# Kernel tuning notes

Hardware: AMD Instinct MI355X
Metric: run time of the kernel (lower is better)

The kernel has to match this reference:

```python
import jax, jax.numpy as jnp
import numpy as np

N_NODES = 50000
N_EDGES = 100000
TOKENS = 10000
D = 32
EDGE_TYPES = 8
STEPS = 5


def setup_inputs() -> dict:
    key = jax.random.key(0)
    ks = jax.random.split(key, 12)
    token = jax.random.randint(ks[0], (N_NODES,), 0, TOKENS)
    etype = jax.random.randint(ks[1], (N_EDGES,), 0, EDGE_TYPES)
    src = jax.random.randint(ks[2], (N_EDGES,), 0, N_NODES)
    dst = jax.random.randint(ks[3], (N_EDGES,), 0, N_NODES)
    s = 1.0 / np.sqrt(D)
    emb = jax.random.normal(ks[4], (TOKENS, D), jnp.float32)
    # per-edge-type weights: [T, D, D, 2] (fwd/reverse message transforms)
    W_edge = jax.random.normal(ks[5], (EDGE_TYPES, D, D, 2), jnp.float32) * s
    W_r = jax.random.normal(ks[6], (3 * D, D), jnp.float32) * s
    b_r = jnp.zeros((D,), jnp.float32)
    W_z = jax.random.normal(ks[7], (3 * D, D), jnp.float32) * s
    b_z = jnp.zeros((D,), jnp.float32)
    W_t = jax.random.normal(ks[8], (3 * D, D), jnp.float32) * s
    b_t = jnp.zeros((D,), jnp.float32)
    return {"token": token, "etype": etype, "src": src, "dst": dst,
            "emb": emb, "W_edge": W_edge, "W_r": W_r, "b_r": b_r,
            "W_z": W_z, "b_z": b_z, "W_t": W_t, "b_t": b_t}


def reference(token, etype, src, dst, emb, W_edge, W_r, b_r, W_z, b_z, W_t, b_t):
    n = token.shape[0]
    prop = emb[token]                       # [N, D]
    We = W_edge[etype]                      # [E, D, D, 2] gathered per edge (once)
    for _ in range(STEPS):
        h_src = prop[src]                   # [E, D] gather source states
        # src_mul_edge + sum over src dim == per-edge matmul: [E,D,2]
        fea = jnp.einsum('ei,eijk->ejk', h_src, We)
        in_fea = jax.ops.segment_sum(fea[:, :, 0], dst, num_segments=n)   # [N, D]
        out_fea = jax.ops.segment_sum(fea[:, :, 1], src, num_segments=n)  # [N, D]
        cat = jnp.concatenate([in_fea, out_fea, prop], axis=1)            # [N, 3D]
        r = jax.nn.sigmoid(cat @ W_r + b_r)
        z = jax.nn.sigmoid(cat @ W_z + b_z)
        cat2 = jnp.concatenate([in_fea, out_fea, r * prop], axis=1)
        h_hat = jnp.tanh(cat2 @ W_t + b_t)
        prop = (1.0 - z) * prop + z * h_hat
    return prop
```

## Files before the change

kernel.cpp:

```cpp
#include <hip/hip_runtime.h>

#define N_NODES 50000
#define N_EDGES 100000
#define DD 32
#define STEPS 5
#define ETYPES 8
#define CAP_T 13312
#define CAP (ETYPES * CAP_T)
#define TRASH N_EDGES
#define SCAN_B 49

#define GRU_GRID ((N_NODES / 16 + 3) / 4)

typedef float f32x4v __attribute__((ext_vector_type(4)));
typedef short s16x8 __attribute__((ext_vector_type(8)));

__device__ __forceinline__ ushort f2bf(float x) {
    unsigned u = __float_as_uint(x);
    u += 0x7fff + ((u >> 16) & 1);
    return (ushort)(u >> 16);
}
__device__ __forceinline__ float bf2f(ushort h) {
    return __uint_as_float(((unsigned)h) << 16);
}
__device__ __forceinline__ void mk_split(const float* v, s16x8& h, s16x8& lo) {
#pragma unroll
    for (int i = 0; i < 8; ++i) {
        ushort hi = f2bf(v[i]);
        h[i] = (short)hi;
        lo[i] = (short)f2bf(v[i] - bf2f(hi));
    }
}
__device__ __forceinline__ float sigm(float x) {
    return 1.f / (1.f + __expf(-x));
}
__device__ __forceinline__ float fast_tanh(float x) {
    x = fminf(fmaxf(x, -15.f), 15.f);
    float e = __expf(2.f * x);
    return (e - 1.f) / (e + 1.f);
}

__global__ void init_kernel(const int* __restrict__ token,
                            const float* __restrict__ emb,
                            float* __restrict__ prop,
                            int* __restrict__ cnt,
                            int* __restrict__ se,
                            int* __restrict__ spi,
                            int* __restrict__ spo) {
    int idx = blockIdx.x * 256 + threadIdx.x;
    int n = idx >> 5, j = idx & 31;
    prop[idx] = emb[token[n] * DD + j];
    if (idx < 2 * N_NODES + ETYPES) cnt[idx] = 0;
    if (idx < CAP) { se[idx] = 0; spi[idx] = TRASH; spo[idx] = TRASH; }
}

__global__ __launch_bounds__(256) void
wfrag_kernel(const float* __restrict__ W_edge,
             ushort* __restrict__ wfh, ushort* __restrict__ wfl) {
    int idx = blockIdx.x * 256 + threadIdx.x;
    if (idx >= ETYPES * 4 * 64) return;
    int t  = idx >> 8;
    int nt = (idx >> 6) & 3;
    int l  = idx & 63;
    int n  = nt * 16 + (l & 15);
    int j  = n & 31;
    int p  = n >> 5;
#pragma unroll
    for (int i = 0; i < 8; ++i) {
        int k = (l >> 4) * 8 + i;
        float v = W_edge[(((size_t)t * DD + k) * DD + j) * 2 + p];
        ushort hi = f2bf(v);
        int o = ((t * 4 + nt) * 64 + l) * 8 + i;
        wfh[o] = hi;
        wfl[o] = f2bf(v - bf2f(hi));
    }
}

__global__ __launch_bounds__(256) void
wgfrag_kernel(const float* __restrict__ W_r, const float* __restrict__ W_z,
              const float* __restrict__ W_t,
              ushort* __restrict__ wgh, ushort* __restrict__ wgl) {
    int idx = blockIdx.x * 256 + threadIdx.x;
    if (idx >= 1152) return;
    int g  = idx / 384;
    int kt = (idx / 128) % 3;
    int nt = (idx / 64) % 2;
    int l  = idx & 63;
    const float* W = g == 0 ? W_r : (g == 1 ? W_z : W_t);
    int col = nt * 16 + (l & 15);
#pragma unroll
    for (int i = 0; i < 8; ++i) {
        int k = kt * 32 + (l >> 4) * 8 + i;
        float v = W[k * DD + col];
        ushort hi = f2bf(v);
        int o = (((g * 3 + kt) * 2 + nt) * 64 + l) * 8 + i;
        wgh[o] = hi;
        wgl[o] = f2bf(v - bf2f(hi));
    }
}

__global__ void hist_kernel(const int* __restrict__ etype,
                            const int* __restrict__ src,
                            const int* __restrict__ dst,
                            int* __restrict__ cnt_in, int* __restrict__ cnt_out,
                            int* __restrict__ tcnt,
                            int* __restrict__ rank_in, int* __restrict__ rank_out,
                            int* __restrict__ qe) {
    __shared__ int lh[ETYPES], lbase[ETYPES];
    int tid = threadIdx.x;
    int e = blockIdx.x * 256 + tid;
    if (tid < ETYPES) lh[tid] = 0;
    __syncthreads();
    int t = 0, lr = 0;
    bool v = e < N_EDGES;
    if (v) {
        t = etype[e];
        lr = atomicAdd(&lh[t], 1);
        rank_in[e]  = atomicAdd(&cnt_in[dst[e]], 1);
        rank_out[e] = atomicAdd(&cnt_out[src[e]], 1);
    }
    __syncthreads();
    if (tid < ETYPES) lbase[tid] = atomicAdd(&tcnt[tid], lh[tid]);
    __syncthreads();
    if (v) qe[e] = t * CAP_T + lbase[t] + lr;
}

__global__ __launch_bounds__(1024) void
scan1(const int* __restrict__ cnt_in, const int* __restrict__ cnt_out,
      int* __restrict__ off_in, int* __restrict__ off_out,
      int* __restrict__ bsum) {
    __shared__ int s[1024];
    int b = blockIdx.x;
    int ab = (b < SCAN_B) ? b : b - SCAN_B;
    const int* a = (b < SCAN_B) ? cnt_in : cnt_out;
    int* o = (b < SCAN_B) ? off_in : off_out;
    int i = ab * 1024 + threadIdx.x;
    int x = (i < N_NODES) ? a[i] : 0;
    s[threadIdx.x] = x;
    __syncthreads();
    for (int ofs = 1; ofs < 1024; ofs <<= 1) {
        int u = (threadIdx.x >= ofs) ? s[threadIdx.x - ofs] : 0;
        __syncthreads();
        s[threadIdx.x] += u;
        __syncthreads();
    }
    if (i < N_NODES) o[i] = s[threadIdx.x] - x;
    if (threadIdx.x == 1023) bsum[b] = s[1023];
}

__global__ void scan2(const int* __restrict__ bsum, int* __restrict__ ebase,
                      int* __restrict__ off_in, int* __restrict__ off_out) {
    __shared__ int s[128];
    int t = threadIdx.x;
    int x = (t < 2 * SCAN_B) ? bsum[t] : 0;
    s[t] = x;
    __syncthreads();
    for (int ofs = 1; ofs < 128; ofs <<= 1) {
        int u = (t >= ofs) ? s[t - ofs] : 0;
        __syncthreads();
        s[t] += u;
        __syncthreads();
    }
    if (t < SCAN_B) ebase[t] = s[t] - x;
    else if (t < 2 * SCAN_B) ebase[t] = s[t] - x - N_EDGES;
    if (t == 0) { off_in[N_NODES] = N_EDGES; off_out[N_NODES] = N_EDGES; }
}

__global__ __launch_bounds__(1024) void
scan3(int* __restrict__ off_in, int* __restrict__ off_out,
      const int* __restrict__ ebase) {
    int b = blockIdx.x;
    int ab = (b < SCAN_B) ? b : b - SCAN_B;
    int* o = (b < SCAN_B) ? off_in : off_out;
    int i = ab * 1024 + threadIdx.x;
    if (i < N_NODES) o[i] += ebase[b];
}

__global__ void place_kernel(const int* __restrict__ src,
                             const int* __restrict__ dst,
                             const int* __restrict__ in_off,
                             const int* __restrict__ out_off,
                             const int* __restrict__ rank_in,
                             const int* __restrict__ rank_out,
                             const int* __restrict__ qe,
                             int* __restrict__ se, int* __restrict__ spi,
                             int* __restrict__ spo) {
    int e = blockIdx.x * 256 + threadIdx.x;
    if (e < N_EDGES) {
        int q = qe[e];
        int pi = in_off[dst[e]]  + rank_in[e];
        int po = out_off[src[e]] + rank_out[e];
        if (q < CAP) {
            se[q]  = src[e];
            spi[q] = pi;
            spo[q] = po;
        }
    }
}

__global__ __launch_bounds__(256) void
edge_kernel(const int* __restrict__ se, const int* __restrict__ spi,
            const int* __restrict__ spo,
            const ushort* __restrict__ wfh, const ushort* __restrict__ wfl,
            const float* __restrict__ prop,
            float* __restrict__ fea_in, float* __restrict__ fea_out) {
    int wv = blockIdx.x * 4 + (threadIdx.x >> 6);
    int l  = threadIdx.x & 63;
    int slot0 = wv * 16;
    int type = slot0 / CAP_T;
    int m  = l & 15;
    int kb = l >> 4;

    int sm = se[slot0 + m];
    const float4* p4 = (const float4*)prop;
    float4 h0 = p4[(size_t)sm * 8 + kb * 2];
    float4 h1 = p4[(size_t)sm * 8 + kb * 2 + 1];
    float hv[8] = {h0.x, h0.y, h0.z, h0.w, h1.x, h1.y, h1.z, h1.w};
    s16x8 ah, al;
    mk_split(hv, ah, al);

    int pr[4], qr[4];
#pragma unroll
    for (int reg = 0; reg < 4; ++reg) {
        pr[reg] = spi[slot0 + kb * 4 + reg];
        qr[reg] = spo[slot0 + kb * 4 + reg];
    }

    const s16x8* bh8 = (const s16x8*)wfh;
    const s16x8* bl8 = (const s16x8*)wfl;
    f32x4v acc[4];
#pragma unroll
    for (int nt = 0; nt < 4; ++nt) {
        s16x8 bh = bh8[(type * 4 + nt) * 64 + l];
        s16x8 bl = bl8[(type * 4 + nt) * 64 + l];
        f32x4v a = {0.f, 0.f, 0.f, 0.f};
        a = __builtin_amdgcn_mfma_f32_16x16x32_bf16(ah, bh, a, 0, 0, 0);
        a = __builtin_amdgcn_mfma_f32_16x16x32_bf16(al, bh, a, 0, 0, 0);
        a = __builtin_amdgcn_mfma_f32_16x16x32_bf16(ah, bl, a, 0, 0, 0);
        acc[nt] = a;
    }

    int col = l & 15;
#pragma unroll
    for (int nt = 0; nt < 4; ++nt) {
        float* base = (nt < 2) ? fea_in : fea_out;
        int cofs = (nt & 1) * 16 + col;
#pragma unroll
        for (int reg = 0; reg < 4; ++reg) {
            int row = (nt < 2) ? pr[reg] : qr[reg];
            base[(size_t)row * DD + cofs] = acc[nt][reg];
        }
    }
}

__global__ __launch_bounds__(256) void
gru_kernel(const ushort* __restrict__ wgh, const ushort* __restrict__ wgl,
           const float* __restrict__ b_r, const float* __restrict__ b_z,
           const float* __restrict__ b_t,
           const float* __restrict__ fea_in,
           const float* __restrict__ fea_out,
           const int* __restrict__ in_off,
           const int* __restrict__ out_off,
           float* __restrict__ prop,
           float* __restrict__ out2) {
    __shared__ float tr[4][16 * 36];
    const int wvl = threadIdx.x >> 6;
    const int wv = blockIdx.x * 4 + wvl;
    if (wv * 16 >= N_NODES) return;
    const int l = threadIdx.x & 63;
    const int m = l & 15;
    const int kb = l >> 4;
    const int gn = wv * 16 + m;

    float va[8], vb[8], pA[8];
    {
        const float4* p4 = (const float4*)prop;
        float4 a = p4[(size_t)gn * 8 + kb * 2];
        float4 b = p4[(size_t)gn * 8 + kb * 2 + 1];
        pA[0] = a.x; pA[1] = a.y; pA[2] = a.z; pA[3] = a.w;
        pA[4] = b.x; pA[5] = b.y; pA[6] = b.z; pA[7] = b.w;
#pragma unroll
        for (int i = 0; i < 8; ++i) { va[i] = 0.f; vb[i] = 0.f; }
        const float4* fi4 = (const float4*)fea_in;
        const float4* fo4 = (const float4*)fea_out;
        int i0 = in_off[gn], i1 = in_off[gn + 1];
        for (int r = i0; r < i1; ++r) {
            float4 x = fi4[(size_t)r * 8 + kb * 2];
            float4 y = fi4[(size_t)r * 8 + kb * 2 + 1];
            va[0] += x.x; va[1] += x.y; va[2] += x.z; va[3] += x.w;
            va[4] += y.x; va[5] += y.y; va[6] += y.z; va[7] += y.w;
        }
        int o0 = out_off[gn], o1 = out_off[gn + 1];
        for (int r = o0; r < o1; ++r) {
            float4 x = fo4[(size_t)r * 8 + kb * 2];
            float4 y = fo4[(size_t)r * 8 + kb * 2 + 1];
            vb[0] += x.x; vb[1] += x.y; vb[2] += x.z; vb[3] += x.w;
            vb[4] += y.x; vb[5] += y.y; vb[6] += y.z; vb[7] += y.w;
        }
    }
    s16x8 ah[3], al[3];
    mk_split(va, ah[0], al[0]);
    mk_split(vb, ah[1], al[1]);
    mk_split(pA, ah[2], al[2]);

    const s16x8* bh8 = (const s16x8*)wgh;
    const s16x8* bl8 = (const s16x8*)wgl;
    f32x4v ar[2], az[2], at_[2];
#pragma unroll
    for (int nt = 0; nt < 2; ++nt) {
        ar[nt] = (f32x4v){0.f, 0.f, 0.f, 0.f};
        az[nt] = (f32x4v){0.f, 0.f, 0.f, 0.f};
        at_[nt] = (f32x4v){0.f, 0.f, 0.f, 0.f};
    }
#pragma unroll
    for (int nt = 0; nt < 2; ++nt) {
#pragma unroll
        for (int kt = 0; kt < 3; ++kt) {
            s16x8 bh = bh8[((0 * 3 + kt) * 2 + nt) * 64 + l];
            s16x8 bl = bl8[((0 * 3 + kt) * 2 + nt) * 64 + l];
            ar[nt] = __builtin_amdgcn_mfma_f32_16x16x32_bf16(ah[kt], bh, ar[nt], 0, 0, 0);
            ar[nt] = __builtin_amdgcn_mfma_f32_16x16x32_bf16(al[kt], bh, ar[nt], 0, 0, 0);
            ar[nt] = __builtin_amdgcn_mfma_f32_16x16x32_bf16(ah[kt], bl, ar[nt], 0, 0, 0);
            s16x8 ch = bh8[((1 * 3 + kt) * 2 + nt) * 64 + l];
            s16x8 cl = bl8[((1 * 3 + kt) * 2 + nt) * 64 + l];
            az[nt] = __builtin_amdgcn_mfma_f32_16x16x32_bf16(ah[kt], ch, az[nt], 0, 0, 0);
            az[nt] = __builtin_amdgcn_mfma_f32_16x16x32_bf16(al[kt], ch, az[nt], 0, 0, 0);
            az[nt] = __builtin_amdgcn_mfma_f32_16x16x32_bf16(ah[kt], cl, az[nt], 0, 0, 0);
            if (kt < 2) {
                s16x8 th = bh8[((2 * 3 + kt) * 2 + nt) * 64 + l];
                s16x8 tl = bl8[((2 * 3 + kt) * 2 + nt) * 64 + l];
                at_[nt] = __builtin_amdgcn_mfma_f32_16x16x32_bf16(ah[kt], th, at_[nt], 0, 0, 0);
                at_[nt] = __builtin_amdgcn_mfma_f32_16x16x32_bf16(al[kt], th, at_[nt], 0, 0, 0);
                at_[nt] = __builtin_amdgcn_mfma_f32_16x16x32_bf16(ah[kt], tl, at_[nt], 0, 0, 0);
            }
        }
    }

    float rv[2][4], zv[2][4], pD[2][4];
#pragma unroll
    for (int nt = 0; nt < 2; ++nt) {
        float br = b_r[nt * 16 + m];
        float bz = b_z[nt * 16 + m];
#pragma unroll
        for (int reg = 0; reg < 4; ++reg) {
            int nd = wv * 16 + kb * 4 + reg;
            pD[nt][reg] = prop[(size_t)nd * DD + nt * 16 + m];
            rv[nt][reg] = sigm(ar[nt][reg] + br) * pD[nt][reg];
            zv[nt][reg] = sigm(az[nt][reg] + bz);
        }
    }

    float* T = tr[wvl];
#pragma unroll
    for (int nt = 0; nt < 2; ++nt)
#pragma unroll
        for (int reg = 0; reg < 4; ++reg)
            T[(kb * 4 + reg) * 36 + nt * 16 + m] = rv[nt][reg];
    float rpA[8];
    {
        const float4* T4 = (const float4*)(T + m * 36 + kb * 8);
        float4 x = T4[0], y = T4[1];
        rpA[0] = x.x; rpA[1] = x.y; rpA[2] = x.z; rpA[3] = x.w;
        rpA[4] = y.x; rpA[5] = y.y; rpA[6] = y.z; rpA[7] = y.w;
    }
    s16x8 rh, rl;
    mk_split(rpA, rh, rl);
#pragma unroll
    for (int nt = 0; nt < 2; ++nt) {
        s16x8 th = bh8[((2 * 3 + 2) * 2 + nt) * 64 + l];
        s16x8 tl = bl8[((2 * 3 + 2) * 2 + nt) * 64 + l];
        at_[nt] = __builtin_amdgcn_mfma_f32_16x16x32_bf16(rh, th, at_[nt], 0, 0, 0);
        at_[nt] = __builtin_amdgcn_mfma_f32_16x16x32_bf16(rl, th, at_[nt], 0, 0, 0);
        at_[nt] = __builtin_amdgcn_mfma_f32_16x16x32_bf16(rh, tl, at_[nt], 0, 0, 0);
    }

#pragma unroll
    for (int nt = 0; nt < 2; ++nt) {
        float bt = b_t[nt * 16 + m];
#pragma unroll
        for (int reg = 0; reg < 4; ++reg) {
            int nd = wv * 16 + kb * 4 + reg;
            float tv = fast_tanh(at_[nt][reg] + bt);
            float o = fmaf(zv[nt][reg], tv - pD[nt][reg], pD[nt][reg]);
            if (out2) out2[(size_t)nd * DD + nt * 16 + m] = o;
            else      prop[(size_t)nd * DD + nt * 16 + m] = o;
        }
    }
}

extern "C" void kernel_launch(void* const* d_in, const int* in_sizes, int n_in,
                              void* d_out, int out_size, void* d_ws, size_t ws_size,
                              hipStream_t stream) {
    const int*   token  = (const int*)d_in[0];
    const int*   etype  = (const int*)d_in[1];
    const int*   src    = (const int*)d_in[2];
    const int*   dst    = (const int*)d_in[3];
    const float* emb    = (const float*)d_in[4];
    const float* W_edge = (const float*)d_in[5];
    const float* W_r    = (const float*)d_in[6];
    const float* b_r    = (const float*)d_in[7];
    const float* W_z    = (const float*)d_in[8];
    const float* b_z    = (const float*)d_in[9];
    const float* W_t    = (const float*)d_in[10];
    const float* b_t    = (const float*)d_in[11];
    float* out = (float*)d_out;

    float* prop    = (float*)d_ws;
    float* fea_in  = prop    + (size_t)N_NODES * DD;
    float* fea_out = fea_in  + (size_t)(N_EDGES + 1) * DD;
    ushort* wfh = (ushort*)(fea_out + (size_t)(N_EDGES + 1) * DD);
    ushort* wfl = wfh + ETYPES * 4 * 64 * 8;
    ushort* wgh = wfl + ETYPES * 4 * 64 * 8;
    ushort* wgl = wgh + 1152 * 8;
    int* in_off   = (int*)(wgl + 1152 * 8);
    int* out_off  = in_off + (N_NODES + 1);
    int* se       = out_off + (N_NODES + 1);
    int* spi      = se + CAP;
    int* spo      = spi + CAP;

    int* cnt      = (int*)fea_in;
    int* cnt_in   = cnt;
    int* cnt_out  = cnt + N_NODES;
    int* tcnt     = cnt + 2 * N_NODES;
    int* rank_in  = cnt + 2 * N_NODES + ETYPES;
    int* rank_out = rank_in + N_EDGES;
    int* qe       = rank_out + N_EDGES;
    int* bsum     = qe + N_EDGES;
    int* ebase    = bsum + 2 * SCAN_B;

    init_kernel<<<(N_NODES * DD) / 256, 256, 0, stream>>>(token, emb, prop, cnt,
                                                          se, spi, spo);
    wfrag_kernel<<<8, 256, 0, stream>>>(W_edge, wfh, wfl);
    wgfrag_kernel<<<5, 256, 0, stream>>>(W_r, W_z, W_t, wgh, wgl);
    hist_kernel<<<(N_EDGES + 255) / 256, 256, 0, stream>>>(
        etype, src, dst, cnt_in, cnt_out, tcnt, rank_in, rank_out, qe);
    scan1<<<2 * SCAN_B, 1024, 0, stream>>>(cnt_in, cnt_out, in_off, out_off, bsum);
    scan2<<<1, 128, 0, stream>>>(bsum, ebase, in_off, out_off);
    scan3<<<2 * SCAN_B, 1024, 0, stream>>>(in_off, out_off, ebase);
    place_kernel<<<(N_EDGES + 255) / 256, 256, 0, stream>>>(
        src, dst, in_off, out_off, rank_in, rank_out, qe, se, spi, spo);

    for (int step = 0; step < STEPS; ++step) {
        edge_kernel<<<CAP / 64, 256, 0, stream>>>(se, spi, spo, wfh, wfl, prop,
                                                  fea_in, fea_out);
        gru_kernel<<<GRU_GRID, 256, 0, stream>>>(
            wgh, wgl, b_r, b_z, b_t, fea_in, fea_out, in_off, out_off,
            prop, (step == STEPS - 1) ? out : nullptr);
    }
}
```

Baseline: 243.6 us.

## Compute outgoing messages per node from per-type out-degree counts instead of per edge

After: 240.5 us. Within noise of the previous version (-1.3%).

```diff
diff --git a/kernel.cpp b/kernel.cpp
--- a/kernel.cpp
+++ b/kernel.cpp
@@ -14,6 +14,7 @@
 
 typedef float f32x4v __attribute__((ext_vector_type(4)));
 typedef short s16x8 __attribute__((ext_vector_type(8)));
+typedef unsigned long long u64;
 
 __device__ __forceinline__ ushort f2bf(float x) {
     unsigned u = __float_as_uint(x);
@@ -44,68 +45,66 @@
                             const float* __restrict__ emb,
                             float* __restrict__ prop,
                             int* __restrict__ cnt,
+                            u64* __restrict__ c8,
                             int* __restrict__ se,
-                            int* __restrict__ spi,
-                            int* __restrict__ spo) {
+                            int* __restrict__ spi) {
     int idx = blockIdx.x * 256 + threadIdx.x;
     int n = idx >> 5, j = idx & 31;
     prop[idx] = emb[token[n] * DD + j];
-    if (idx < 2 * N_NODES + ETYPES) cnt[idx] = 0;
-    if (idx < CAP) { se[idx] = 0; spi[idx] = TRASH; spo[idx] = TRASH; }
+    if (idx < N_NODES + ETYPES) cnt[idx] = 0;
+    if (idx < N_NODES) c8[idx] = 0ull;
+    if (idx < CAP) { se[idx] = 0; spi[idx] = TRASH; }
 }
 
 __global__ __launch_bounds__(256) void
 wfrag_kernel(const float* __restrict__ W_edge,
-             ushort* __restrict__ wfh, ushort* __restrict__ wfl) {
+             const float* __restrict__ W_r, const float* __restrict__ W_z,
+             const float* __restrict__ W_t,
+             ushort* __restrict__ wfh, ushort* __restrict__ wfl,
+             ushort* __restrict__ wgh, ushort* __restrict__ wgl) {
     int idx = blockIdx.x * 256 + threadIdx.x;
-    if (idx >= ETYPES * 4 * 64) return;
-    int t  = idx >> 8;
-    int nt = (idx >> 6) & 3;
-    int l  = idx & 63;
-    int n  = nt * 16 + (l & 15);
-    int j  = n & 31;
-    int p  = n >> 5;
-#pragma unroll
-    for (int i = 0; i < 8; ++i) {
-        int k = (l >> 4) * 8 + i;
-        float v = W_edge[(((size_t)t * DD + k) * DD + j) * 2 + p];
-        ushort hi = f2bf(v);
-        int o = ((t * 4 + nt) * 64 + l) * 8 + i;
-        wfh[o] = hi;
-        wfl[o] = f2bf(v - bf2f(hi));
-    }
-}
-
-__global__ __launch_bounds__(256) void
-wgfrag_kernel(const float* __restrict__ W_r, const float* __restrict__ W_z,
-              const float* __restrict__ W_t,
-              ushort* __restrict__ wgh, ushort* __restrict__ wgl) {
-    int idx = blockIdx.x * 256 + threadIdx.x;
-    if (idx >= 1152) return;
-    int g  = idx / 384;
-    int kt = (idx / 128) % 3;
-    int nt = (idx / 64) % 2;
-    int l  = idx & 63;
-    const float* W = g == 0 ? W_r : (g == 1 ? W_z : W_t);
-    int col = nt * 16 + (l & 15);
-#pragma unroll
-    for (int i = 0; i < 8; ++i) {
-        int k = kt * 32 + (l >> 4) * 8 + i;
-        float v = W[k * DD + col];
-        ushort hi = f2bf(v);
-        int o = (((g * 3 + kt) * 2 + nt) * 64 + l) * 8 + i;
-        wgh[o] = hi;
-        wgl[o] = f2bf(v - bf2f(hi));
+    if (idx < ETYPES * 4 * 64) {
+        int t  = idx >> 8;
+        int nt = (idx >> 6) & 3;
+        int l  = idx & 63;
+        int n  = nt * 16 + (l & 15);
+        int j  = n & 31;
+        int p  = n >> 5;
+#pragma unroll
+        for (int i = 0; i < 8; ++i) {
+            int k = (l >> 4) * 8 + i;
+            float v = W_edge[(((size_t)t * DD + k) * DD + j) * 2 + p];
+            ushort hi = f2bf(v);
+            int o = ((t * 4 + nt) * 64 + l) * 8 + i;
+            wfh[o] = hi;
+            wfl[o] = f2bf(v - bf2f(hi));
+        }
+    } else if (idx < ETYPES * 4 * 64 + 1152) {
+        int x = idx - ETYPES * 4 * 64;
+        int g  = x / 384;
+        int kt = (x / 128) % 3;
+        int nt = (x / 64) % 2;
+        int l  = x & 63;
+        const float* W = g == 0 ? W_r : (g == 1 ? W_z : W_t);
+        int col = nt * 16 + (l & 15);
+#pragma unroll
+        for (int i = 0; i < 8; ++i) {
+            int k = kt * 32 + (l >> 4) * 8 + i;
+            float v = W[k * DD + col];
+            ushort hi = f2bf(v);
+            int o = (((g * 3 + kt) * 2 + nt) * 64 + l) * 8 + i;
+            wgh[o] = hi;
+            wgl[o] = f2bf(v - bf2f(hi));
+        }
     }
 }
 
 __global__ void hist_kernel(const int* __restrict__ etype,
                             const int* __restrict__ src,
                             const int* __restrict__ dst,
-                            int* __restrict__ cnt_in, int* __restrict__ cnt_out,
-                            int* __restrict__ tcnt,
-                            int* __restrict__ rank_in, int* __restrict__ rank_out,
-                            int* __restrict__ qe) {
+                            int* __restrict__ cnt_in, int* __restrict__ tcnt,
+                            u64* __restrict__ c8,
+                            int* __restrict__ rank_in, int* __restrict__ qe) {
     __shared__ int lh[ETYPES], lbase[ETYPES];
     int tid = threadIdx.x;
     int e = blockIdx.x * 256 + tid;
@@ -116,8 +115,8 @@
     if (v) {
         t = etype[e];
         lr = atomicAdd(&lh[t], 1);
-        rank_in[e]  = atomicAdd(&cnt_in[dst[e]], 1);
-        rank_out[e] = atomicAdd(&cnt_out[src[e]], 1);
+        rank_in[e] = atomicAdd(&cnt_in[dst[e]], 1);
+        atomicAdd(&c8[src[e]], 1ull << (8 * t));
     }
     __syncthreads();
     if (tid < ETYPES) lbase[tid] = atomicAdd(&tcnt[tid], lh[tid]);
@@ -126,16 +125,11 @@
 }
 
 __global__ __launch_bounds__(1024) void
-scan1(const int* __restrict__ cnt_in, const int* __restrict__ cnt_out,
-      int* __restrict__ off_in, int* __restrict__ off_out,
+scan1(const int* __restrict__ cnt_in, int* __restrict__ off_in,
       int* __restrict__ bsum) {
     __shared__ int s[1024];
-    int b = blockIdx.x;
-    int ab = (b < SCAN_B) ? b : b - SCAN_B;
-    const int* a = (b < SCAN_B) ? cnt_in : cnt_out;
-    int* o = (b < SCAN_B) ? off_in : off_out;
-    int i = ab * 1024 + threadIdx.x;
-    int x = (i < N_NODES) ? a[i] : 0;
+    int i = blockIdx.x * 1024 + threadIdx.x;
+    int x = (i < N_NODES) ? cnt_in[i] : 0;
     s[threadIdx.x] = x;
     __syncthreads();
     for (int ofs = 1; ofs < 1024; ofs <<= 1) {
@@ -144,66 +138,54 @@
         s[threadIdx.x] += u;
         __syncthreads();
     }
-    if (i < N_NODES) o[i] = s[threadIdx.x] - x;
-    if (threadIdx.x == 1023) bsum[b] = s[1023];
+    if (i < N_NODES) off_in[i] = s[threadIdx.x] - x;
+    if (threadIdx.x == 1023) bsum[blockIdx.x] = s[1023];
 }
 
 __global__ void scan2(const int* __restrict__ bsum, int* __restrict__ ebase,
-                      int* __restrict__ off_in, int* __restrict__ off_out) {
-    __shared__ int s[128];
+                      int* __restrict__ off_in) {
+    __shared__ int s[64];
     int t = threadIdx.x;
-    int x = (t < 2 * SCAN_B) ? bsum[t] : 0;
+    int x = (t < SCAN_B) ? bsum[t] : 0;
     s[t] = x;
     __syncthreads();
-    for (int ofs = 1; ofs < 128; ofs <<= 1) {
+    for (int ofs = 1; ofs < 64; ofs <<= 1) {
         int u = (t >= ofs) ? s[t - ofs] : 0;
         __syncthreads();
         s[t] += u;
         __syncthreads();
     }
     if (t < SCAN_B) ebase[t] = s[t] - x;
-    else if (t < 2 * SCAN_B) ebase[t] = s[t] - x - N_EDGES;
-    if (t == 0) { off_in[N_NODES] = N_EDGES; off_out[N_NODES] = N_EDGES; }
+    if (t == 0) off_in[N_NODES] = N_EDGES;
 }
 
 __global__ __launch_bounds__(1024) void
-scan3(int* __restrict__ off_in, int* __restrict__ off_out,
-      const int* __restrict__ ebase) {
-    int b = blockIdx.x;
-    int ab = (b < SCAN_B) ? b : b - SCAN_B;
-    int* o = (b < SCAN_B) ? off_in : off_out;
-    int i = ab * 1024 + threadIdx.x;
-    if (i < N_NODES) o[i] += ebase[b];
+scan3(int* __restrict__ off_in, const int* __restrict__ ebase) {
+    int i = blockIdx.x * 1024 + threadIdx.x;
+    if (i < N_NODES) off_in[i] += ebase[blockIdx.x];
 }
 
 __global__ void place_kernel(const int* __restrict__ src,
                              const int* __restrict__ dst,
                              const int* __restrict__ in_off,
-                             const int* __restrict__ out_off,
                              const int* __restrict__ rank_in,
-                             const int* __restrict__ rank_out,
                              const int* __restrict__ qe,
-                             int* __restrict__ se, int* __restrict__ spi,
-                             int* __restrict__ spo) {
+                             int* __restrict__ se, int* __restrict__ spi) {
     int e = blockIdx.x * 256 + threadIdx.x;
     if (e < N_EDGES) {
         int q = qe[e];
-        int pi = in_off[dst[e]]  + rank_in[e];
-        int po = out_off[src[e]] + rank_out[e];
         if (q < CAP) {
             se[q]  = src[e];
-            spi[q] = pi;
-            spo[q] = po;
+            spi[q] = in_off[dst[e]] + rank_in[e];
         }
     }
 }
 
 __global__ __launch_bounds__(256) void
 edge_kernel(const int* __restrict__ se, const int* __restrict__ spi,
-            const int* __restrict__ spo,
             const ushort* __restrict__ wfh, const ushort* __restrict__ wfl,
             const float* __restrict__ prop,
-            float* __restrict__ fea_in, float* __restrict__ fea_out) {
+            float* __restrict__ fea_in) {
     int wv = blockIdx.x * 4 + (threadIdx.x >> 6);
     int l  = threadIdx.x & 63;
     int slot0 = wv * 16;
@@ -219,18 +201,15 @@
     s16x8 ah, al;
     mk_split(hv, ah, al);
 
-    int pr[4], qr[4];
-#pragma unroll
-    for (int reg = 0; reg < 4; ++reg) {
-        pr[reg] = spi[slot0 + kb * 4 + reg];
-        qr[reg] = spo[slot0 + kb * 4 + reg];
-    }
+    int pr[4];
+#pragma unroll
+    for (int reg = 0; reg < 4; ++reg) pr[reg] = spi[slot0 + kb * 4 + reg];
 
     const s16x8* bh8 = (const s16x8*)wfh;
     const s16x8* bl8 = (const s16x8*)wfl;
-    f32x4v acc[4];
-#pragma unroll
-    for (int nt = 0; nt < 4; ++nt) {
+    f32x4v acc[2];
+#pragma unroll
+    for (int nt = 0; nt < 2; ++nt) {
         s16x8 bh = bh8[(type * 4 + nt) * 64 + l];
         s16x8 bl = bl8[(type * 4 + nt) * 64 + l];
         f32x4v a = {0.f, 0.f, 0.f, 0.f};
@@ -239,28 +218,21 @@
         a = __builtin_amdgcn_mfma_f32_16x16x32_bf16(ah, bl, a, 0, 0, 0);
         acc[nt] = a;
     }
-
-    int col = l & 15;
-#pragma unroll
-    for (int nt = 0; nt < 4; ++nt) {
-        float* base = (nt < 2) ? fea_in : fea_out;
-        int cofs = (nt & 1) * 16 + col;
-#pragma unroll
-        for (int reg = 0; reg < 4; ++reg) {
-            int row = (nt < 2) ? pr[reg] : qr[reg];
-            base[(size_t)row * DD + cofs] = acc[nt][reg];
-        }
-    }
+#pragma unroll
+    for (int nt = 0; nt < 2; ++nt)
+#pragma unroll
+        for (int reg = 0; reg < 4; ++reg)
+            fea_in[(size_t)pr[reg] * DD + nt * 16 + m] = acc[nt][reg];
 }
 
 __global__ __launch_bounds__(256) void
 gru_kernel(const ushort* __restrict__ wgh, const ushort* __restrict__ wgl,
+           const ushort* __restrict__ wfh, const ushort* __restrict__ wfl,
            const float* __restrict__ b_r, const float* __restrict__ b_z,
            const float* __restrict__ b_t,
            const float* __restrict__ fea_in,
-           const float* __restrict__ fea_out,
            const int* __restrict__ in_off,
-           const int* __restrict__ out_off,
+           const u64* __restrict__ c8,
            float* __restrict__ prop,
            float* __restrict__ out2) {
     __shared__ float tr[4][16 * 36];
@@ -272,7 +244,7 @@
     const int kb = l >> 4;
     const int gn = wv * 16 + m;
 
-    float va[8], vb[8], pA[8];
+    float va[8], pA[8];
     {
         const float4* p4 = (const float4*)prop;
         float4 a = p4[(size_t)gn * 8 + kb * 2];
@@ -280,9 +252,8 @@
         pA[0] = a.x; pA[1] = a.y; pA[2] = a.z; pA[3] = a.w;
         pA[4] = b.x; pA[5] = b.y; pA[6] = b.z; pA[7] = b.w;
 #pragma unroll
-        for (int i = 0; i < 8; ++i) { va[i] = 0.f; vb[i] = 0.f; }
+        for (int i = 0; i < 8; ++i) va[i] = 0.f;
         const float4* fi4 = (const float4*)fea_in;
-        const float4* fo4 = (const float4*)fea_out;
         int i0 = in_off[gn], i1 = in_off[gn + 1];
         for (int r = i0; r < i1; ++r) {
             float4 x = fi4[(size_t)r * 8 + kb * 2];
@@ -290,18 +261,57 @@
             va[0] += x.x; va[1] += x.y; va[2] += x.z; va[3] += x.w;
             va[4] += y.x; va[5] += y.y; va[6] += y.z; va[7] += y.w;
         }
-        int o0 = out_off[gn], o1 = out_off[gn + 1];
-        for (int r = o0; r < o1; ++r) {
-            float4 x = fo4[(size_t)r * 8 + kb * 2];
-            float4 y = fo4[(size_t)r * 8 + kb * 2 + 1];
-            vb[0] += x.x; vb[1] += x.y; vb[2] += x.z; vb[3] += x.w;
-            vb[4] += y.x; vb[5] += y.y; vb[6] += y.z; vb[7] += y.w;
-        }
-    }
+    }
+    s16x8 ph, pl;
+    mk_split(pA, ph, pl);
+
+    u64 cb[4];
+#pragma unroll
+    for (int reg = 0; reg < 4; ++reg) cb[reg] = c8[wv * 16 + kb * 4 + reg];
+    const s16x8* eh8 = (const s16x8*)wfh;
+    const s16x8* el8 = (const s16x8*)wfl;
+    f32x4v outD[2];
+    outD[0] = (f32x4v){0.f, 0.f, 0.f, 0.f};
+    outD[1] = (f32x4v){0.f, 0.f, 0.f, 0.f};
+#pragma unroll 1
+    for (int t = 0; t < ETYPES; ++t) {
+        s16x8 bh2 = eh8[(t * 4 + 2) * 64 + l];
+        s16x8 bl2 = el8[(t * 4 + 2) * 64 + l];
+        s16x8 bh3 = eh8[(t * 4 + 3) * 64 + l];
+        s16x8 bl3 = el8[(t * 4 + 3) * 64 + l];
+        f32x4v a0 = {0.f, 0.f, 0.f, 0.f}, a1 = {0.f, 0.f, 0.f, 0.f};
+        a0 = __builtin_amdgcn_mfma_f32_16x16x32_bf16(ph, bh2, a0, 0, 0, 0);
+        a0 = __builtin_amdgcn_mfma_f32_16x16x32_bf16(pl, bh2, a0, 0, 0, 0);
+        a0 = __builtin_amdgcn_mfma_f32_16x16x32_bf16(ph, bl2, a0, 0, 0, 0);
+        a1 = __builtin_amdgcn_mfma_f32_16x16x32_bf16(ph, bh3, a1, 0, 0, 0);
+        a1 = __builtin_amdgcn_mfma_f32_16x16x32_bf16(pl, bh3, a1, 0, 0, 0);
+        a1 = __builtin_amdgcn_mfma_f32_16x16x32_bf16(ph, bl3, a1, 0, 0, 0);
+#pragma unroll
+        for (int reg = 0; reg < 4; ++reg) {
+            float w = (float)((cb[reg] >> (8 * t)) & 0xff);
+            outD[0][reg] = fmaf(w, a0[reg], outD[0][reg]);
+            outD[1][reg] = fmaf(w, a1[reg], outD[1][reg]);
+        }
+    }
+
+    float* T = tr[wvl];
+#pragma unroll
+    for (int nt = 0; nt < 2; ++nt)
+#pragma unroll
+        for (int reg = 0; reg < 4; ++reg)
+            T[(kb * 4 + reg) * 36 + nt * 16 + m] = outD[nt][reg];
+    float oA[8];
+    {
+        const float4* T4 = (const float4*)(T + m * 36 + kb * 8);
+        float4 x = T4[0], y = T4[1];
+        oA[0] = x.x; oA[1] = x.y; oA[2] = x.z; oA[3] = x.w;
+        oA[4] = y.x; oA[5] = y.y; oA[6] = y.z; oA[7] = y.w;
+    }
+
     s16x8 ah[3], al[3];
     mk_split(va, ah[0], al[0]);
-    mk_split(vb, ah[1], al[1]);
-    mk_split(pA, ah[2], al[2]);
+    mk_split(oA, ah[1], al[1]);
+    ah[2] = ph; al[2] = pl;
 
     const s16x8* bh8 = (const s16x8*)wgh;
     const s16x8* bl8 = (const s16x8*)wgl;
@@ -350,7 +360,6 @@
         }
     }
 
-    float* T = tr[wvl];
 #pragma unroll
     for (int nt = 0; nt < 2; ++nt)
 #pragma unroll
@@ -407,44 +416,40 @@
 
     float* prop    = (float*)d_ws;
     float* fea_in  = prop    + (size_t)N_NODES * DD;
-    float* fea_out = fea_in  + (size_t)(N_EDGES + 1) * DD;
-    ushort* wfh = (ushort*)(fea_out + (size_t)(N_EDGES + 1) * DD);
+    ushort* wfh = (ushort*)(fea_in + (size_t)(N_EDGES + 1) * DD);
     ushort* wfl = wfh + ETYPES * 4 * 64 * 8;
     ushort* wgh = wfl + ETYPES * 4 * 64 * 8;
     ushort* wgl = wgh + 1152 * 8;
-    int* in_off   = (int*)(wgl + 1152 * 8);
-    int* out_off  = in_off + (N_NODES + 1);
-    int* se       = out_off + (N_NODES + 1);
+    u64* c8     = (u64*)(wgl + 1152 * 8);
+    int* in_off   = (int*)(c8 + N_NODES);
+    int* se       = in_off + (N_NODES + 1);
     int* spi      = se + CAP;
-    int* spo      = spi + CAP;
 
     int* cnt      = (int*)fea_in;
     int* cnt_in   = cnt;
-    int* cnt_out  = cnt + N_NODES;
-    int* tcnt     = cnt + 2 * N_NODES;
-    int* rank_in  = cnt + 2 * N_NODES + ETYPES;
-    int* rank_out = rank_in + N_EDGES;
-    int* qe       = rank_out + N_EDGES;
+    int* tcnt     = cnt + N_NODES;
+    int* rank_in  = cnt + N_NODES + ETYPES;
+    int* qe       = rank_in + N_EDGES;
     int* bsum     = qe + N_EDGES;
-    int* ebase    = bsum + 2 * SCAN_B;
+    int* ebase    = bsum + SCAN_B;
 
     init_kernel<<<(N_NODES * DD) / 256, 256, 0, stream>>>(token, emb, prop, cnt,
-                                                          se, spi, spo);
-    wfrag_kernel<<<8, 256, 0, stream>>>(W_edge, wfh, wfl);
-    wgfrag_kernel<<<5, 256, 0, stream>>>(W_r, W_z, W_t, wgh, wgl);
+                                                          c8, se, spi);
+    wfrag_kernel<<<13, 256, 0, stream>>>(W_edge, W_r, W_z, W_t,
+                                         wfh, wfl, wgh, wgl);
     hist_kernel<<<(N_EDGES + 255) / 256, 256, 0, stream>>>(
-        etype, src, dst, cnt_in, cnt_out, tcnt, rank_in, rank_out, qe);
-    scan1<<<2 * SCAN_B, 1024, 0, stream>>>(cnt_in, cnt_out, in_off, out_off, bsum);
-    scan2<<<1, 128, 0, stream>>>(bsum, ebase, in_off, out_off);
-    scan3<<<2 * SCAN_B, 1024, 0, stream>>>(in_off, out_off, ebase);
+        etype, src, dst, cnt_in, tcnt, c8, rank_in, qe);
+    scan1<<<SCAN_B, 1024, 0, stream>>>(cnt_in, in_off, bsum);
+    scan2<<<1, 64, 0, stream>>>(bsum, ebase, in_off);
+    scan3<<<SCAN_B, 1024, 0, stream>>>(in_off, ebase);
     place_kernel<<<(N_EDGES + 255) / 256, 256, 0, stream>>>(
-        src, dst, in_off, out_off, rank_in, rank_out, qe, se, spi, spo);
+        src, dst, in_off, rank_in, qe, se, spi);
 
     for (int step = 0; step < STEPS; ++step) {
-        edge_kernel<<<CAP / 64, 256, 0, stream>>>(se, spi, spo, wfh, wfl, prop,
-                                                  fea_in, fea_out);
+        edge_kernel<<<CAP / 64, 256, 0, stream>>>(se, spi, wfh, wfl, prop,
+                                                  fea_in);
         gru_kernel<<<GRU_GRID, 256, 0, stream>>>(
-            wgh, wgl, b_r, b_z, b_t, fea_in, fea_out, in_off, out_off,
+            wgh, wgl, wfh, wfl, b_r, b_z, b_t, fea_in, in_off, c8,
             prop, (step == STEPS - 1) ? out : nullptr);
     }
 }
```
